# Kernel tuning notes

Measured on AMD Instinct MI355X. Metric: run time of the kernel, lower is better.

Reference implementation:

```python
import jax, jax.numpy as jnp
import numpy as np

BATCH = 10000
NUM_TREES = 1000
NUM_NODES = 511  # full binary tree of depth 8
N_FEATURES = 256
N_CLASSES = 1
MAX_DEPTH = 8


def setup_inputs() -> dict:
    key = jax.random.key(0)
    k = jax.random.split(key, 6)
    flat = NUM_TREES * NUM_NODES
    x = jax.random.normal(k[0], (BATCH, N_FEATURES), dtype=jnp.float32)
    thresholds = jax.random.normal(k[1], (flat,), dtype=jnp.float32)
    values = jax.random.normal(k[2], (flat, N_CLASSES), dtype=jnp.float32)
    lefts = jax.random.randint(k[3], (flat,), 0, NUM_NODES).astype(jnp.int64)
    rights = jax.random.randint(k[4], (flat,), 0, NUM_NODES).astype(jnp.int64)
    features = jax.random.randint(k[5], (flat,), 0, N_FEATURES).astype(jnp.int64)
    return {
        "x": x,
        "thresholds": thresholds,
        "values": values,
        "lefts": lefts,
        "rights": rights,
        "features": features,
        "num_trees": NUM_TREES,
        "num_nodes": NUM_NODES,
        "max_depth": MAX_DEPTH,
    }


def reference(x, thresholds, values, lefts, rights, features, num_trees, num_nodes, max_depth):
    batch = x.shape[0]
    # nodes_offset: flat index of each tree's root in the concatenated node arrays
    nodes_offset = (jnp.arange(num_trees, dtype=jnp.int32) * num_nodes)[None, :]  # [1, T]
    indexes = jnp.broadcast_to(nodes_offset, (batch, num_trees))  # [B, T]
    for _ in range(max_depth):
        feature_nodes = features[indexes]                     # [B, T] feature id per current node
        feature_values = jnp.take_along_axis(x, feature_nodes, axis=1)  # [B, T]
        thr = thresholds[indexes]                             # [B, T]
        l = lefts[indexes]                                    # [B, T]
        r = rights[indexes]                                   # [B, T]
        indexes = jnp.where(feature_values >= thr, r, l) + nodes_offset
    output = values[indexes]  # [B, T, C]
    return output
```

## Files before the change

### kernel.cpp

```cpp
#include <hip/hip_runtime.h>
#include <stdint.h>

#define BATCH     10000
#define NUM_TREES 1000
#define NUM_NODES 511
#define NFEAT     256
#define DEPTH     8
#define FLAT_NODES (NUM_TREES * NUM_NODES)

#define TREE_BYTES 1360
#define VLEAF_OFF  ((size_t)NUM_TREES * TREE_BYTES)
#define WS_NEEDED  (VLEAF_OFF + (size_t)NUM_TREES * 256 * 4)
#define XT_LD      10048
#define XT_OFF     WS_NEEDED
#define XT_BYTES   ((size_t)NFEAT * XT_LD * 4)
#define WS_XT      (XT_OFF + XT_BYTES)

#define BT 64
#define TT 64
#define NTHREADS 1024
#define XS_BYTES  (NFEAT * 64 * 4)
#define OUT_LD    36
#define OS_BYTES  (64 * OUT_LD * 4)
#define SH_BYTES  (XS_BYTES + OS_BYTES)

#define UNROLL_BLOCKS 250
#define TRANS_BLOCKS  (157 * 4)

__device__ __forceinline__ void glds16(const void* g, void* l) {
  __builtin_amdgcn_global_load_lds(
      (const __attribute__((address_space(1))) unsigned int*)g,
      (__attribute__((address_space(3))) unsigned int*)l, 16, 0, 0);
}

__global__ __launch_bounds__(256)
void prepack_kernel(const float* __restrict__ thr,
                    const int* __restrict__ feats,
                    const int* __restrict__ lefts,
                    const int* __restrict__ rights,
                    const float* __restrict__ values,
                    const float* __restrict__ x,
                    unsigned char* __restrict__ ws) {
  __shared__ unsigned char sh[64 * 65 * 4];
  const int tid = threadIdx.x;

  if (blockIdx.x < UNROLL_BLOCKS) {
    uint16_t* n_s = (uint16_t*)sh;
    const int wv = tid >> 6, lane = tid & 63;
    const int tree = blockIdx.x * 4 + wv;
    const int base = tree * NUM_NODES;
    uint16_t* n = n_s + wv * 512;
    uint4* rec   = (uint4*)(ws + (size_t)tree * TREE_BYTES);
    float* vleaf = (float*)(ws + VLEAF_OFF + (size_t)tree * 1024);

    if (lane == 0) n[0] = 0;
    __syncthreads();
    const int EBASE[4] = {0, 1, 5, 21};
    #pragma unroll
    for (int d = 0; d < 8; ++d) {
      const int lvl = (1 << d) - 1, cnt = 1 << d;
      for (int i = lane; i < cnt; i += 64) {
        int p  = lvl + i;
        int np = n[p];
        int nl = lefts[base + np], nr = rights[base + np];
        n[2 * p + 1] = (uint16_t)nl;
        n[2 * p + 2] = (uint16_t)nr;
        if ((d & 1) == 0) {
          uint32_t f3 = (uint32_t)feats[base + np] |
                        ((uint32_t)feats[base + nl] << 8) |
                        ((uint32_t)feats[base + nr] << 16);
          rec[EBASE[d >> 1] + i] =
              make_uint4(__float_as_uint(thr[base + np]),
                         __float_as_uint(thr[base + nl]),
                         __float_as_uint(thr[base + nr]), f3);
        }
      }
      __syncthreads();
    }
    #pragma unroll
    for (int i = lane; i < 256; i += 64)
      vleaf[i] = values[base + n[255 + i]];
  } else {
    float (*tile)[65] = (float(*)[65])sh;
    float* xT = (float*)(ws + XT_OFF);
    const int t = blockIdx.x - UNROLL_BLOCKS;
    const int b0 = (t >> 2) * 64, f0 = (t & 3) * 64;
    const float4* xg = (const float4*)x;
    #pragma unroll
    for (int p = 0; p < 4; ++p) {
      int i = tid + p * 256;
      int r = i >> 4, c4 = i & 15;
      int gb = b0 + r;
      float4 v = (gb < BATCH) ? xg[(size_t)gb * 64 + (f0 >> 2) + c4]
                              : make_float4(0.f, 0.f, 0.f, 0.f);
      tile[r][4 * c4 + 0] = v.x;
      tile[r][4 * c4 + 1] = v.y;
      tile[r][4 * c4 + 2] = v.z;
      tile[r][4 * c4 + 3] = v.w;
    }
    __syncthreads();
    #pragma unroll
    for (int p = 0; p < 4; ++p) {
      int i = tid + p * 256;
      int fr = i >> 4, b4 = i & 15;
      float4 w = make_float4(tile[4 * b4 + 0][fr], tile[4 * b4 + 1][fr],
                             tile[4 * b4 + 2][fr], tile[4 * b4 + 3][fr]);
      *(float4*)(xT + (size_t)(f0 + fr) * XT_LD + b0 + 4 * b4) = w;
    }
  }
}

template <bool XT>
__global__ __launch_bounds__(NTHREADS, 8)
void traverse64(const float* __restrict__ x,
                const unsigned char* __restrict__ ws,
                float* __restrict__ out) {
  extern __shared__ unsigned char smem[];
  float* x_s   = (float*)smem;
  float* out_s = (float*)(smem + XS_BYTES);

  const int tid  = threadIdx.x;
  const int wid  = tid >> 6;
  const int lane = tid & 63;
  const int b0   = blockIdx.y * BT;
  const int t0   = blockIdx.x * TT;

  const unsigned char* nb = ws + (size_t)(t0 + 4 * wid) * TREE_BYTES;
  uint4 r[4];
  #pragma unroll
  for (int c = 0; c < 4; ++c)
    r[c] = *(const uint4*)(nb + (size_t)c * TREE_BYTES);

  if (XT) {
    const float* xT = (const float*)(ws + XT_OFF);
    #pragma unroll
    for (int k = 0; k < 4; ++k) {
      int fi = tid + k * NTHREADS;
      int f = fi >> 4, c16 = fi & 15;
      glds16(xT + (size_t)f * XT_LD + b0 + 4 * c16,
             (unsigned char*)x_s + (size_t)fi * 16);
    }
  } else {
    const float4* xg = (const float4*)x;
    #pragma unroll
    for (int p = 0; p < 4; ++p) {
      int i = tid + p * NTHREADS;
      int rr = i >> 6, c = i & 63;
      int gb = b0 + rr;
      float4 v = (gb < BATCH) ? xg[(size_t)gb * 64 + c]
                              : make_float4(0.f, 0.f, 0.f, 0.f);
      int o = (c << 8) + (rr ^ (c & 31));
      x_s[o]       = v.x;
      x_s[o + 64]  = v.y;
      x_s[o + 128] = v.z;
      x_s[o + 192] = v.w;
    }
  }
  __syncthreads();

  auto xgather = [&](int f) -> float {
    if (XT) return x_s[(f << 6) + lane];
    return x_s[(f << 6) + (lane ^ ((f >> 2) & 31))];
  };

  int loc[4] = {0, 0, 0, 0};
  #pragma unroll
  for (int it = 0; it < 4; ++it) {
    float xp[4], xl[4], xr[4];
    #pragma unroll
    for (int c = 0; c < 4; ++c) {
      xp[c] = xgather(r[c].w & 255);
      xl[c] = xgather((r[c].w >> 8) & 255);
      xr[c] = xgather((r[c].w >> 16) & 255);
    }
    #pragma unroll
    for (int c = 0; c < 4; ++c) {
      bool c0  = (xp[c] >= __uint_as_float(r[c].x));
      float xc = c0 ? xr[c] : xl[c];
      float tc = __uint_as_float(c0 ? r[c].z : r[c].y);
      loc[c] = 4 * loc[c] + 2 * (int)c0 + (int)(xc >= tc);
    }
    if (it < 3) {
      const int eoff = (it == 0) ? 16 : (it == 1) ? 80 : 336;
      #pragma unroll
      for (int c = 0; c < 4; ++c)
        r[c] = *(const uint4*)(nb + (size_t)c * TREE_BYTES + loc[c] * 16 + eoff);
    }
  }
  const float* vl = (const float*)(ws + VLEAF_OFF);
  float4 v;
  {
    const int gt0 = t0 + 4 * wid;
    int g0 = (gt0 + 0 < NUM_TREES) ? gt0 + 0 : 0;
    int g1 = (gt0 + 1 < NUM_TREES) ? gt0 + 1 : 0;
    int g2 = (gt0 + 2 < NUM_TREES) ? gt0 + 2 : 0;
    int g3 = (gt0 + 3 < NUM_TREES) ? gt0 + 3 : 0;
    v = make_float4(vl[(size_t)g0 * 256 + loc[0]],
                    vl[(size_t)g1 * 256 + loc[1]],
                    vl[(size_t)g2 * 256 + loc[2]],
                    vl[(size_t)g3 * 256 + loc[3]]);
  }

  if (wid < 8)
    *(float4*)(out_s + lane * OUT_LD + 4 * wid) = v;
  __syncthreads();
  {
    int col = tid & 31, rr = tid >> 5;
    #pragma unroll
    for (int k = 0; k < 2; ++k) {
      int row = rr + 32 * k;
      int gb = b0 + row, gt = t0 + col;
      if (gb < BATCH && gt < NUM_TREES)
        out[(size_t)gb * NUM_TREES + gt] = out_s[row * OUT_LD + col];
    }
  }
  __syncthreads();
  if (wid >= 8)
    *(float4*)(out_s + lane * OUT_LD + 4 * (wid - 8)) = v;
  __syncthreads();
  {
    int col = tid & 31, rr = tid >> 5;
    #pragma unroll
    for (int k = 0; k < 2; ++k) {
      int row = rr + 32 * k;
      int gb = b0 + row, gt = t0 + 32 + col;
      if (gb < BATCH && gt < NUM_TREES)
        out[(size_t)gb * NUM_TREES + gt] = out_s[row * OUT_LD + col];
    }
  }
}

#define FB_BT 64
#define FB_TT 64
#define FB_TPR 16
#define FB_NROUNDS 4
#define FB_NTHREADS 1024
#define FB_XS (NFEAT * 64 * 4)
#define FB_NSU (FB_TPR * NUM_NODES)
#define FB_NS (FB_NSU * 8)
#define FB_OLD (FB_TT + 1)
#define FB_OS (FB_BT * FB_OLD * 4)
#define FB_SH (FB_XS + FB_NS + FB_OS)
#define FB_PREF ((FB_NSU + FB_NTHREADS - 1) / FB_NTHREADS)

__global__ __launch_bounds__(FB_NTHREADS, 1)
void fb_traverse(const float* __restrict__ x,
                 const float* __restrict__ thrg,
                 const int* __restrict__ featg,
                 const int* __restrict__ leftg,
                 const int* __restrict__ rightg,
                 const float* __restrict__ values,
                 float* __restrict__ out) {
  extern __shared__ unsigned char smem[];
  float* x_s     = (float*)smem;
  uint2* nodes_s = (uint2*)(smem + FB_XS);
  float* out_s   = (float*)(smem + FB_XS + FB_NS);
  const int tid = threadIdx.x, wid = tid >> 6, lane = tid & 63;
  const int b0 = blockIdx.y * FB_BT, t0 = blockIdx.x * FB_TT;
  uint2 pf[FB_PREF];
  auto load_round = [&](int rr) {
    const int gbase = (t0 + rr * FB_TPR) * NUM_NODES;
    #pragma unroll
    for (int k = 0; k < FB_PREF; ++k) {
      int fi = tid + k * FB_NTHREADS;
      uint2 v = make_uint2(0u, 0u);
      if (fi < FB_NSU) {
        int gi = gbase + fi;
        if (gi < FLAT_NODES) {
          uint32_t meta = (uint32_t)featg[gi] | ((uint32_t)leftg[gi] << 8) |
                          ((uint32_t)rightg[gi] << 20);
          v = make_uint2(__float_as_uint(thrg[gi]), meta);
        }
      }
      pf[k] = v;
    }
  };
  auto write_nodes = [&]() {
    #pragma unroll
    for (int k = 0; k < FB_PREF; ++k) {
      int fi = tid + k * FB_NTHREADS;
      if (fi < FB_NSU) nodes_s[fi] = pf[k];
    }
  };
  load_round(0);
  {
    const float4* xg = (const float4*)x;
    #pragma unroll
    for (int p = 0; p < (FB_BT * (NFEAT / 4)) / FB_NTHREADS; ++p) {
      int i = tid + p * FB_NTHREADS;
      int r = i >> 6, c = i & 63;
      int gb = b0 + r;
      float4 v = make_float4(0.f, 0.f, 0.f, 0.f);
      if (gb < BATCH) v = xg[gb * (NFEAT / 4) + c];
      int o = (c << 8) + (r ^ (c & 31));
      x_s[o] = v.x; x_s[o + 64] = v.y; x_s[o + 128] = v.z; x_s[o + 192] = v.w;
    }
  }
  write_nodes();
  __syncthreads();
  for (int r = 0; r < FB_NROUNDS; ++r) {
    if (r + 1 < FB_NROUNDS) load_round(r + 1);
    const uint2* nA = nodes_s + wid * NUM_NODES;
    const int tr0 = t0 + r * FB_TPR;
    const int gta = tr0 + wid;
    const int offA = (gta < NUM_TREES ? gta : 0) * NUM_NODES;
    uint2 na = nA[0];
    float va = 0.f;
    #pragma unroll
    for (int d = 0; d < DEPTH; ++d) {
      int fa = na.y & 0xFF;
      int la = (na.y >> 8) & 0xFFF;
      int ra = (int)(na.y >> 20);
      float xa = x_s[(fa << 6) + (lane ^ ((fa >> 2) & 31))];
      if (d < DEPTH - 1) {
        uint2 nla = nA[la], nra = nA[ra];
        na = (xa >= __uint_as_float(na.x)) ? nra : nla;
      } else {
        float vla = values[offA + la], vra = values[offA + ra];
        va = (xa >= __uint_as_float(na.x)) ? vra : vla;
      }
    }
    out_s[lane * FB_OLD + r * FB_TPR + wid] = va;
    __syncthreads();
    if (r + 1 < FB_NROUNDS) { write_nodes(); __syncthreads(); }
  }
  {
    const int gt = t0 + lane;
    #pragma unroll
    for (int p = 0; p < FB_BT / 16; ++p) {
      int rr = p * 16 + wid;
      int gb = b0 + rr;
      if (gb < BATCH && gt < NUM_TREES)
        out[gb * NUM_TREES + gt] = out_s[rr * FB_OLD + lane];
    }
  }
}

extern "C" void kernel_launch(void* const* d_in, const int* in_sizes, int n_in,
                              void* d_out, int out_size, void* d_ws, size_t ws_size,
                              hipStream_t stream) {
  const float* x          = (const float*)d_in[0];
  const float* thresholds = (const float*)d_in[1];
  const float* values     = (const float*)d_in[2];
  const int*   lefts      = (const int*)d_in[3];
  const int*   rights     = (const int*)d_in[4];
  const int*   features   = (const int*)d_in[5];
  float* out = (float*)d_out;

  if (ws_size >= WS_XT) {
    unsigned char* ws = (unsigned char*)d_ws;
    prepack_kernel<<<UNROLL_BLOCKS + TRANS_BLOCKS, 256, 0, stream>>>(
        thresholds, features, lefts, rights, values, x, ws);
    hipFuncSetAttribute(reinterpret_cast<const void*>(traverse64<true>),
                        hipFuncAttributeMaxDynamicSharedMemorySize, SH_BYTES);
    dim3 grid((NUM_TREES + TT - 1) / TT, (BATCH + BT - 1) / BT);
    traverse64<true><<<grid, NTHREADS, SH_BYTES, stream>>>(x, ws, out);
  } else if (ws_size >= WS_NEEDED) {
    unsigned char* ws = (unsigned char*)d_ws;
    prepack_kernel<<<UNROLL_BLOCKS, 256, 0, stream>>>(
        thresholds, features, lefts, rights, values, x, ws);
    hipFuncSetAttribute(reinterpret_cast<const void*>(traverse64<false>),
                        hipFuncAttributeMaxDynamicSharedMemorySize, SH_BYTES);
    dim3 grid((NUM_TREES + TT - 1) / TT, (BATCH + BT - 1) / BT);
    traverse64<false><<<grid, NTHREADS, SH_BYTES, stream>>>(x, ws, out);
  } else {
    hipFuncSetAttribute(reinterpret_cast<const void*>(fb_traverse),
                        hipFuncAttributeMaxDynamicSharedMemorySize, FB_SH);
    dim3 grid((NUM_TREES + FB_TT - 1) / FB_TT, (BATCH + FB_BT - 1) / FB_BT);
    fb_traverse<<<grid, FB_NTHREADS, FB_SH, stream>>>(
        x, thresholds, features, lefts, rights, values, out);
  }
}
```

Measured before the change: 55.10 us.

## Process two batch tiles per block, prefetch next x tile, gather only chosen child

Each block now handles two consecutive 64-row batch tiles. It reuses the tree root loads and restages the next x tile into shared memory while the current tile's output is written. The traversal now gathers only the child feature selected by the first comparison instead of both children. The final level loads a float2 leaf pair and selects between them, instead of doing a dependent leaf load after traversal. Together these cut redundant shared-memory reads and halve the grid, at the cost of more serialization per block and fewer blocks to hide latency.

```diff
diff --git a/kernel.cpp b/kernel.cpp
--- a/kernel.cpp
+++ b/kernel.cpp
@@ -18,6 +18,7 @@
 
 #define BT 64
 #define TT 64
+#define YT 2
 #define NTHREADS 1024
 #define XS_BYTES  (NFEAT * 64 * 4)
 #define OUT_LD    36
@@ -122,111 +123,148 @@
   const int tid  = threadIdx.x;
   const int wid  = tid >> 6;
   const int lane = tid & 63;
-  const int b0   = blockIdx.y * BT;
+  const int bbase = blockIdx.y * (YT * BT);
   const int t0   = blockIdx.x * TT;
 
   const unsigned char* nb = ws + (size_t)(t0 + 4 * wid) * TREE_BYTES;
-  uint4 r[4];
+  uint4 rinit[4];
   #pragma unroll
   for (int c = 0; c < 4; ++c)
-    r[c] = *(const uint4*)(nb + (size_t)c * TREE_BYTES);
-
-  if (XT) {
-    const float* xT = (const float*)(ws + XT_OFF);
-    #pragma unroll
-    for (int k = 0; k < 4; ++k) {
-      int fi = tid + k * NTHREADS;
-      int f = fi >> 4, c16 = fi & 15;
-      glds16(xT + (size_t)f * XT_LD + b0 + 4 * c16,
-             (unsigned char*)x_s + (size_t)fi * 16);
-    }
-  } else {
-    const float4* xg = (const float4*)x;
-    #pragma unroll
-    for (int p = 0; p < 4; ++p) {
-      int i = tid + p * NTHREADS;
-      int rr = i >> 6, c = i & 63;
-      int gb = b0 + rr;
-      float4 v = (gb < BATCH) ? xg[(size_t)gb * 64 + c]
-                              : make_float4(0.f, 0.f, 0.f, 0.f);
-      int o = (c << 8) + (rr ^ (c & 31));
-      x_s[o]       = v.x;
-      x_s[o + 64]  = v.y;
-      x_s[o + 128] = v.z;
-      x_s[o + 192] = v.w;
-    }
-  }
-  __syncthreads();
-
+    rinit[c] = *(const uint4*)(nb + (size_t)c * TREE_BYTES);
+
+  const float* vl = (const float*)(ws + VLEAF_OFF);
+  int gcl[4];
+  #pragma unroll
+  for (int c = 0; c < 4; ++c) {
+    int g = t0 + 4 * wid + c;
+    gcl[c] = (g < NUM_TREES) ? g : 0;
+  }
+
+  auto stage = [&](int b0) {
+    if (XT) {
+      const float* xT = (const float*)(ws + XT_OFF);
+      #pragma unroll
+      for (int k = 0; k < 4; ++k) {
+        int fi = tid + k * NTHREADS;
+        int f = fi >> 4, c16 = fi & 15;
+        glds16(xT + (size_t)f * XT_LD + b0 + 4 * c16,
+               (unsigned char*)x_s + (size_t)fi * 16);
+      }
+    } else {
+      const float4* xg = (const float4*)x;
+      #pragma unroll
+      for (int p = 0; p < 4; ++p) {
+        int i = tid + p * NTHREADS;
+        int rr = i >> 6, cc = i & 63;
+        int gb = b0 + rr;
+        float4 v = (gb < BATCH) ? xg[(size_t)gb * 64 + cc]
+                                : make_float4(0.f, 0.f, 0.f, 0.f);
+        int o = (cc << 8) + (rr ^ (cc & 31));
+        x_s[o]       = v.x;
+        x_s[o + 64]  = v.y;
+        x_s[o + 128] = v.z;
+        x_s[o + 192] = v.w;
+      }
+    }
+  };
   auto xgather = [&](int f) -> float {
     if (XT) return x_s[(f << 6) + lane];
     return x_s[(f << 6) + (lane ^ ((f >> 2) & 31))];
   };
 
-  int loc[4] = {0, 0, 0, 0};
-  #pragma unroll
-  for (int it = 0; it < 4; ++it) {
-    float xp[4], xl[4], xr[4];
-    #pragma unroll
-    for (int c = 0; c < 4; ++c) {
-      xp[c] = xgather(r[c].w & 255);
-      xl[c] = xgather((r[c].w >> 8) & 255);
-      xr[c] = xgather((r[c].w >> 16) & 255);
-    }
-    #pragma unroll
-    for (int c = 0; c < 4; ++c) {
-      bool c0  = (xp[c] >= __uint_as_float(r[c].x));
-      float xc = c0 ? xr[c] : xl[c];
-      float tc = __uint_as_float(c0 ? r[c].z : r[c].y);
-      loc[c] = 4 * loc[c] + 2 * (int)c0 + (int)(xc >= tc);
-    }
-    if (it < 3) {
+  stage(bbase);
+  __syncthreads();
+
+  for (int yt = 0; yt < YT; ++yt) {
+    const int b0 = bbase + yt * BT;
+    if (b0 >= BATCH) break;
+
+    uint4 r[4];
+    #pragma unroll
+    for (int c = 0; c < 4; ++c) r[c] = rinit[c];
+    int loc[4] = {0, 0, 0, 0};
+    #pragma unroll
+    for (int it = 0; it < 3; ++it) {
+      float xp[4];
+      #pragma unroll
+      for (int c = 0; c < 4; ++c)
+        xp[c] = xgather(r[c].w & 255);
+      bool c0[4]; int fc[4]; float tc[4];
+      #pragma unroll
+      for (int c = 0; c < 4; ++c) {
+        c0[c] = (xp[c] >= __uint_as_float(r[c].x));
+        fc[c] = c0[c] ? ((r[c].w >> 16) & 255) : ((r[c].w >> 8) & 255);
+        tc[c] = __uint_as_float(c0[c] ? r[c].z : r[c].y);
+      }
+      float xc[4];
+      #pragma unroll
+      for (int c = 0; c < 4; ++c)
+        xc[c] = xgather(fc[c]);
+      #pragma unroll
+      for (int c = 0; c < 4; ++c)
+        loc[c] = 4 * loc[c] + 2 * (int)c0[c] + (int)(xc[c] >= tc[c]);
       const int eoff = (it == 0) ? 16 : (it == 1) ? 80 : 336;
       #pragma unroll
       for (int c = 0; c < 4; ++c)
         r[c] = *(const uint4*)(nb + (size_t)c * TREE_BYTES + loc[c] * 16 + eoff);
     }
-  }
-  const float* vl = (const float*)(ws + VLEAF_OFF);
-  float4 v;
-  {
-    const int gt0 = t0 + 4 * wid;
-    int g0 = (gt0 + 0 < NUM_TREES) ? gt0 + 0 : 0;
-    int g1 = (gt0 + 1 < NUM_TREES) ? gt0 + 1 : 0;
-    int g2 = (gt0 + 2 < NUM_TREES) ? gt0 + 2 : 0;
-    int g3 = (gt0 + 3 < NUM_TREES) ? gt0 + 3 : 0;
-    v = make_float4(vl[(size_t)g0 * 256 + loc[0]],
-                    vl[(size_t)g1 * 256 + loc[1]],
-                    vl[(size_t)g2 * 256 + loc[2]],
-                    vl[(size_t)g3 * 256 + loc[3]]);
-  }
-
-  if (wid < 8)
-    *(float4*)(out_s + lane * OUT_LD + 4 * wid) = v;
-  __syncthreads();
-  {
-    int col = tid & 31, rr = tid >> 5;
-    #pragma unroll
-    for (int k = 0; k < 2; ++k) {
-      int row = rr + 32 * k;
-      int gb = b0 + row, gt = t0 + col;
-      if (gb < BATCH && gt < NUM_TREES)
-        out[(size_t)gb * NUM_TREES + gt] = out_s[row * OUT_LD + col];
-    }
-  }
-  __syncthreads();
-  if (wid >= 8)
-    *(float4*)(out_s + lane * OUT_LD + 4 * (wid - 8)) = v;
-  __syncthreads();
-  {
-    int col = tid & 31, rr = tid >> 5;
-    #pragma unroll
-    for (int k = 0; k < 2; ++k) {
-      int row = rr + 32 * k;
-      int gb = b0 + row, gt = t0 + 32 + col;
-      if (gb < BATCH && gt < NUM_TREES)
-        out[(size_t)gb * NUM_TREES + gt] = out_s[row * OUT_LD + col];
-    }
+    float v[4];
+    {
+      float xp[4];
+      #pragma unroll
+      for (int c = 0; c < 4; ++c)
+        xp[c] = xgather(r[c].w & 255);
+      bool c0[4]; int fc[4]; float tc[4]; float2 lf[4];
+      #pragma unroll
+      for (int c = 0; c < 4; ++c) {
+        c0[c] = (xp[c] >= __uint_as_float(r[c].x));
+        fc[c] = c0[c] ? ((r[c].w >> 16) & 255) : ((r[c].w >> 8) & 255);
+        tc[c] = __uint_as_float(c0[c] ? r[c].z : r[c].y);
+        lf[c] = *(const float2*)(vl + (size_t)gcl[c] * 256 +
+                                 4 * loc[c] + 2 * (int)c0[c]);
+      }
+      float xc[4];
+      #pragma unroll
+      for (int c = 0; c < 4; ++c)
+        xc[c] = xgather(fc[c]);
+      #pragma unroll
+      for (int c = 0; c < 4; ++c)
+        v[c] = (xc[c] >= tc[c]) ? lf[c].y : lf[c].x;
+    }
+    float4 V = make_float4(v[0], v[1], v[2], v[3]);
+
+    __syncthreads();
+    if (yt + 1 < YT && bbase + BT < BATCH)
+      stage(bbase + BT);
+
+    if (wid < 8)
+      *(float4*)(out_s + lane * OUT_LD + 4 * wid) = V;
+    __syncthreads();
+    {
+      int col = tid & 31, rr = tid >> 5;
+      #pragma unroll
+      for (int k = 0; k < 2; ++k) {
+        int row = rr + 32 * k;
+        int gb = b0 + row, gt = t0 + col;
+        if (gb < BATCH && gt < NUM_TREES)
+          out[(size_t)gb * NUM_TREES + gt] = out_s[row * OUT_LD + col];
+      }
+    }
+    __syncthreads();
+    if (wid >= 8)
+      *(float4*)(out_s + lane * OUT_LD + 4 * (wid - 8)) = V;
+    __syncthreads();
+    {
+      int col = tid & 31, rr = tid >> 5;
+      #pragma unroll
+      for (int k = 0; k < 2; ++k) {
+        int row = rr + 32 * k;
+        int gb = b0 + row, gt = t0 + 32 + col;
+        if (gb < BATCH && gt < NUM_TREES)
+          out[(size_t)gb * NUM_TREES + gt] = out_s[row * OUT_LD + col];
+      }
+    }
+    if (yt + 1 < YT) __syncthreads();
   }
 }
 
@@ -347,13 +385,14 @@
   const int*   features   = (const int*)d_in[5];
   float* out = (float*)d_out;
 
+  const int nbt = (BATCH + BT - 1) / BT;
   if (ws_size >= WS_XT) {
     unsigned char* ws = (unsigned char*)d_ws;
     prepack_kernel<<<UNROLL_BLOCKS + TRANS_BLOCKS, 256, 0, stream>>>(
         thresholds, features, lefts, rights, values, x, ws);
     hipFuncSetAttribute(reinterpret_cast<const void*>(traverse64<true>),
                         hipFuncAttributeMaxDynamicSharedMemorySize, SH_BYTES);
-    dim3 grid((NUM_TREES + TT - 1) / TT, (BATCH + BT - 1) / BT);
+    dim3 grid((NUM_TREES + TT - 1) / TT, (nbt + YT - 1) / YT);
     traverse64<true><<<grid, NTHREADS, SH_BYTES, stream>>>(x, ws, out);
   } else if (ws_size >= WS_NEEDED) {
     unsigned char* ws = (unsigned char*)d_ws;
@@ -361,7 +400,7 @@
         thresholds, features, lefts, rights, values, x, ws);
     hipFuncSetAttribute(reinterpret_cast<const void*>(traverse64<false>),
                         hipFuncAttributeMaxDynamicSharedMemorySize, SH_BYTES);
-    dim3 grid((NUM_TREES + TT - 1) / TT, (BATCH + BT - 1) / BT);
+    dim3 grid((NUM_TREES + TT - 1) / TT, (nbt + YT - 1) / YT);
     traverse64<false><<<grid, NTHREADS, SH_BYTES, stream>>>(x, ws, out);
   } else {
     hipFuncSetAttribute(reinterpret_cast<const void*>(fb_traverse),
```

New measurement: 66.84 us. 21.3% more time.

## Halve batch tile to 32 rows and alias the output staging buffer onto x tile

Applied to the files above, without the earlier changes.

The traversal kernel now covers 32 batch rows per block with 512 threads. Each wave splits into two half-waves that walk different trees over the same 32 rows. The output transpose buffer reuses the x shared-memory tile after a barrier, which cuts LDS per block to 32 KB and drops the max-dynamic-shared-memory attribute calls. The aim is more resident blocks and fewer host-side API calls per launch. The cost is that each x tile is reused across half as many trees' worth of batch rows, the grid doubles, and half-waves that read different features may hit LDS bank conflicts.

```diff
diff --git a/kernel.cpp b/kernel.cpp
--- a/kernel.cpp
+++ b/kernel.cpp
@@ -16,13 +16,12 @@
 #define XT_BYTES   ((size_t)NFEAT * XT_LD * 4)
 #define WS_XT      (XT_OFF + XT_BYTES)
 
-#define BT 64
+#define BT 32
 #define TT 64
-#define NTHREADS 1024
-#define XS_BYTES  (NFEAT * 64 * 4)
-#define OUT_LD    36
-#define OS_BYTES  (64 * OUT_LD * 4)
-#define SH_BYTES  (XS_BYTES + OS_BYTES)
+#define NTHREADS 512
+#define XS_BYTES  (NFEAT * BT * 4)
+#define OUT_LD    67
+#define SH_BYTES  XS_BYTES
 
 #define UNROLL_BLOCKS 250
 #define TRANS_BLOCKS  (157 * 4)
@@ -112,31 +111,33 @@
 
 template <bool XT>
 __global__ __launch_bounds__(NTHREADS, 8)
-void traverse64(const float* __restrict__ x,
+void traverse32(const float* __restrict__ x,
                 const unsigned char* __restrict__ ws,
                 float* __restrict__ out) {
   extern __shared__ unsigned char smem[];
   float* x_s   = (float*)smem;
-  float* out_s = (float*)(smem + XS_BYTES);
+  float* out_s = (float*)smem;
 
   const int tid  = threadIdx.x;
   const int wid  = tid >> 6;
   const int lane = tid & 63;
+  const int row  = lane & 31;
+  const int th   = lane >> 5;
   const int b0   = blockIdx.y * BT;
   const int t0   = blockIdx.x * TT;
 
-  const unsigned char* nb = ws + (size_t)(t0 + 4 * wid) * TREE_BYTES;
+  const unsigned char* nb = ws + (size_t)(t0 + 8 * wid + th) * TREE_BYTES;
   uint4 r[4];
   #pragma unroll
-  for (int c = 0; c < 4; ++c)
-    r[c] = *(const uint4*)(nb + (size_t)c * TREE_BYTES);
+  for (int s = 0; s < 4; ++s)
+    r[s] = *(const uint4*)(nb + (size_t)(2 * s) * TREE_BYTES);
 
   if (XT) {
     const float* xT = (const float*)(ws + XT_OFF);
     #pragma unroll
     for (int k = 0; k < 4; ++k) {
       int fi = tid + k * NTHREADS;
-      int f = fi >> 4, c16 = fi & 15;
+      int f = fi >> 3, c16 = fi & 7;
       glds16(xT + (size_t)f * XT_LD + b0 + 4 * c16,
              (unsigned char*)x_s + (size_t)fi * 16);
     }
@@ -149,18 +150,18 @@
       int gb = b0 + rr;
       float4 v = (gb < BATCH) ? xg[(size_t)gb * 64 + c]
                               : make_float4(0.f, 0.f, 0.f, 0.f);
-      int o = (c << 8) + (rr ^ (c & 31));
-      x_s[o]       = v.x;
-      x_s[o + 64]  = v.y;
-      x_s[o + 128] = v.z;
-      x_s[o + 192] = v.w;
+      int o = (c << 7) + (rr ^ (c & 31));
+      x_s[o]      = v.x;
+      x_s[o + 32] = v.y;
+      x_s[o + 64] = v.z;
+      x_s[o + 96] = v.w;
     }
   }
   __syncthreads();
 
   auto xgather = [&](int f) -> float {
-    if (XT) return x_s[(f << 6) + lane];
-    return x_s[(f << 6) + (lane ^ ((f >> 2) & 31))];
+    if (XT) return x_s[(f << 5) + row];
+    return x_s[(f << 5) + (row ^ ((f >> 2) & 31))];
   };
 
   int loc[4] = {0, 0, 0, 0};
@@ -168,65 +169,48 @@
   for (int it = 0; it < 4; ++it) {
     float xp[4], xl[4], xr[4];
     #pragma unroll
-    for (int c = 0; c < 4; ++c) {
-      xp[c] = xgather(r[c].w & 255);
-      xl[c] = xgather((r[c].w >> 8) & 255);
-      xr[c] = xgather((r[c].w >> 16) & 255);
-    }
-    #pragma unroll
-    for (int c = 0; c < 4; ++c) {
-      bool c0  = (xp[c] >= __uint_as_float(r[c].x));
-      float xc = c0 ? xr[c] : xl[c];
-      float tc = __uint_as_float(c0 ? r[c].z : r[c].y);
-      loc[c] = 4 * loc[c] + 2 * (int)c0 + (int)(xc >= tc);
+    for (int s = 0; s < 4; ++s) {
+      xp[s] = xgather(r[s].w & 255);
+      xl[s] = xgather((r[s].w >> 8) & 255);
+      xr[s] = xgather((r[s].w >> 16) & 255);
+    }
+    #pragma unroll
+    for (int s = 0; s < 4; ++s) {
+      bool c0  = (xp[s] >= __uint_as_float(r[s].x));
+      float xc = c0 ? xr[s] : xl[s];
+      float tc = __uint_as_float(c0 ? r[s].z : r[s].y);
+      loc[s] = 4 * loc[s] + 2 * (int)c0 + (int)(xc >= tc);
     }
     if (it < 3) {
       const int eoff = (it == 0) ? 16 : (it == 1) ? 80 : 336;
       #pragma unroll
-      for (int c = 0; c < 4; ++c)
-        r[c] = *(const uint4*)(nb + (size_t)c * TREE_BYTES + loc[c] * 16 + eoff);
+      for (int s = 0; s < 4; ++s)
+        r[s] = *(const uint4*)(nb + (size_t)(2 * s) * TREE_BYTES +
+                               loc[s] * 16 + eoff);
     }
   }
   const float* vl = (const float*)(ws + VLEAF_OFF);
-  float4 v;
-  {
-    const int gt0 = t0 + 4 * wid;
-    int g0 = (gt0 + 0 < NUM_TREES) ? gt0 + 0 : 0;
-    int g1 = (gt0 + 1 < NUM_TREES) ? gt0 + 1 : 0;
-    int g2 = (gt0 + 2 < NUM_TREES) ? gt0 + 2 : 0;
-    int g3 = (gt0 + 3 < NUM_TREES) ? gt0 + 3 : 0;
-    v = make_float4(vl[(size_t)g0 * 256 + loc[0]],
-                    vl[(size_t)g1 * 256 + loc[1]],
-                    vl[(size_t)g2 * 256 + loc[2]],
-                    vl[(size_t)g3 * 256 + loc[3]]);
-  }
-
-  if (wid < 8)
-    *(float4*)(out_s + lane * OUT_LD + 4 * wid) = v;
+  float v[4];
+  #pragma unroll
+  for (int s = 0; s < 4; ++s) {
+    int g  = t0 + 8 * wid + 2 * s + th;
+    int cg = (g < NUM_TREES) ? g : 0;
+    v[s] = vl[(size_t)cg * 256 + loc[s]];
+  }
+
   __syncthreads();
-  {
-    int col = tid & 31, rr = tid >> 5;
-    #pragma unroll
-    for (int k = 0; k < 2; ++k) {
-      int row = rr + 32 * k;
-      int gb = b0 + row, gt = t0 + col;
-      if (gb < BATCH && gt < NUM_TREES)
-        out[(size_t)gb * NUM_TREES + gt] = out_s[row * OUT_LD + col];
-    }
-  }
+  #pragma unroll
+  for (int s = 0; s < 4; ++s)
+    out_s[row * OUT_LD + 8 * wid + 2 * s + th] = v[s];
   __syncthreads();
-  if (wid >= 8)
-    *(float4*)(out_s + lane * OUT_LD + 4 * (wid - 8)) = v;
-  __syncthreads();
-  {
-    int col = tid & 31, rr = tid >> 5;
-    #pragma unroll
-    for (int k = 0; k < 2; ++k) {
-      int row = rr + 32 * k;
-      int gb = b0 + row, gt = t0 + 32 + col;
-      if (gb < BATCH && gt < NUM_TREES)
-        out[(size_t)gb * NUM_TREES + gt] = out_s[row * OUT_LD + col];
-    }
+
+  #pragma unroll
+  for (int k = 0; k < 4; ++k) {
+    int rr = (tid >> 6) + 8 * k;
+    int col = tid & 63;
+    int gb = b0 + rr, gt = t0 + col;
+    if (gb < BATCH && gt < NUM_TREES)
+      out[(size_t)gb * NUM_TREES + gt] = out_s[rr * OUT_LD + col];
   }
 }
 
@@ -347,27 +331,22 @@
   const int*   features   = (const int*)d_in[5];
   float* out = (float*)d_out;
 
+  dim3 grid((NUM_TREES + TT - 1) / TT, (BATCH + BT - 1) / BT);
   if (ws_size >= WS_XT) {
     unsigned char* ws = (unsigned char*)d_ws;
     prepack_kernel<<<UNROLL_BLOCKS + TRANS_BLOCKS, 256, 0, stream>>>(
         thresholds, features, lefts, rights, values, x, ws);
-    hipFuncSetAttribute(reinterpret_cast<const void*>(traverse64<true>),
-                        hipFuncAttributeMaxDynamicSharedMemorySize, SH_BYTES);
-    dim3 grid((NUM_TREES + TT - 1) / TT, (BATCH + BT - 1) / BT);
-    traverse64<true><<<grid, NTHREADS, SH_BYTES, stream>>>(x, ws, out);
+    traverse32<true><<<grid, NTHREADS, SH_BYTES, stream>>>(x, ws, out);
   } else if (ws_size >= WS_NEEDED) {
     unsigned char* ws = (unsigned char*)d_ws;
     prepack_kernel<<<UNROLL_BLOCKS, 256, 0, stream>>>(
         thresholds, features, lefts, rights, values, x, ws);
-    hipFuncSetAttribute(reinterpret_cast<const void*>(traverse64<false>),
-                        hipFuncAttributeMaxDynamicSharedMemorySize, SH_BYTES);
-    dim3 grid((NUM_TREES + TT - 1) / TT, (BATCH + BT - 1) / BT);
-    traverse64<false><<<grid, NTHREADS, SH_BYTES, stream>>>(x, ws, out);
+    traverse32<false><<<grid, NTHREADS, SH_BYTES, stream>>>(x, ws, out);
   } else {
     hipFuncSetAttribute(reinterpret_cast<const void*>(fb_traverse),
                         hipFuncAttributeMaxDynamicSharedMemorySize, FB_SH);
-    dim3 grid((NUM_TREES + FB_TT - 1) / FB_TT, (BATCH + FB_BT - 1) / FB_BT);
-    fb_traverse<<<grid, FB_NTHREADS, FB_SH, stream>>>(
+    dim3 fgrid((NUM_TREES + FB_TT - 1) / FB_TT, (BATCH + FB_BT - 1) / FB_BT);
+    fb_traverse<<<fgrid, FB_NTHREADS, FB_SH, stream>>>(
         x, thresholds, features, lefts, rights, values, out);
   }
 }
```

After: 55.48 us. About the same (+0.7%).
